# Performance work log

Hardware: AMD Instinct MI355X
Metric: run time of the kernel (lower is better)

The kernel has to match this reference:

```python
import jax, jax.numpy as jnp
import numpy as np

IN_F, OUT_F, BATCH = 4096, 11008, 8

def setup_inputs() -> dict:
    key = jax.random.key(0)
    k_x, k_s, k_sg, k_b = jax.random.split(key, 4)
    x = jax.random.normal(k_x, (BATCH, IN_F), dtype=jnp.float32)
    # stored codes in [1, 255] as in QINSCodec.encode (uint8 storage)
    stored = jax.random.randint(k_s, (OUT_F, IN_F), 1, 256, dtype=jnp.int32).astype(jnp.uint8)
    # sign in {-1, +1} (int8 storage)
    sign = (jax.random.randint(k_sg, (OUT_F, IN_F), 0, 2, dtype=jnp.int32) * 2 - 1).astype(jnp.int8)
    log_min = jnp.array([-10.0], dtype=jnp.float32)
    log_max = jnp.array([0.0], dtype=jnp.float32)
    bias = jax.random.normal(k_b, (OUT_F,), dtype=jnp.float32) * 0.02
    return {"x": x, "stored": stored, "sign": sign, "log_min": log_min, "log_max": log_max, "bias": bias}

def _decode(stored, sign, log_min, log_max):
    # QINSCodec.decode: normalized = (255 - stored)/254; w = sign * exp(log_min + normalized*(log_max-log_min))
    normalized = (255.0 - stored.astype(jnp.float32)) / 254.0
    log_w = log_min + normalized * (log_max - log_min)
    return sign.astype(jnp.float32) * jnp.exp(log_w)

def reference(x, stored, sign, log_min, log_max, bias):
    lmin = log_min[0]
    lmax = log_max[0]
    w = _decode(stored, sign, lmin, lmax)            # [OUT_F, IN_F]
    return x @ w.T + bias                            # F.linear(x, w, bias)
```

## Files before the change

kernel.cpp:

```cpp
#include <hip/hip_runtime.h>
#include <stdint.h>

#define IN_F   4096
#define OUT_F  11008
#define BATCH  8
#define RPW    4
#define WAVES  2
#define RPB    (RPW*WAVES)
#define CHUNK  256

__device__ __forceinline__ float qins_decode(int code, int sgn, float d0, float d1) {
    const float e = __builtin_amdgcn_exp2f(fmaf((float)code, d1, d0));
    const uint32_t m = ((uint32_t)sgn) & 0x80000000u;
    return __uint_as_float(__float_as_uint(e) ^ m);
}

__global__ __launch_bounds__(WAVES*64, 4)
void qins_linear_kernel(const float* __restrict__ x,
                        const int*   __restrict__ stored,
                        const int*   __restrict__ sign,
                        const float* __restrict__ log_min,
                        const float* __restrict__ log_max,
                        const float* __restrict__ bias,
                        float* __restrict__ out)
{
    const int lane = threadIdx.x & 63;
    const int wave = threadIdx.x >> 6;
    const int o0   = blockIdx.x * RPB + wave * RPW;

    const float lmin = log_min[0];
    const float lmax = log_max[0];
    const float L2E  = 1.44269504088896340736f;
    const float d1 = -(lmax - lmin) * (L2E / 254.0f);
    const float d0 = (lmin + (lmax - lmin) * (255.0f / 254.0f)) * L2E;

    float acc[RPW][BATCH];
#pragma unroll
    for (int r = 0; r < RPW; ++r)
#pragma unroll
        for (int b = 0; b < BATCH; ++b) acc[r][b] = 0.0f;

    const int ii0 = lane * 4;

    for (int i0 = 0; i0 < IN_F; i0 += CHUNK) {
        const int ii = i0 + ii0;

        float4 xr[BATCH];
#pragma unroll
        for (int b = 0; b < BATCH; ++b)
            xr[b] = *reinterpret_cast<const float4*>(x + b * IN_F + ii);

        int4 sc[RPW], sg[RPW];
#pragma unroll
        for (int r = 0; r < RPW; ++r) {
            const size_t off = (size_t)(o0 + r) * IN_F + ii;
            sc[r] = *reinterpret_cast<const int4*>(stored + off);
            sg[r] = *reinterpret_cast<const int4*>(sign + off);
        }

#pragma unroll
        for (int r = 0; r < RPW; ++r) {
            const float w0 = qins_decode(sc[r].x, sg[r].x, d0, d1);
            const float w1 = qins_decode(sc[r].y, sg[r].y, d0, d1);
            const float w2 = qins_decode(sc[r].z, sg[r].z, d0, d1);
            const float w3 = qins_decode(sc[r].w, sg[r].w, d0, d1);
#pragma unroll
            for (int b = 0; b < BATCH; ++b) {
                float a = acc[r][b];
                a = fmaf(w0, xr[b].x, a);
                a = fmaf(w1, xr[b].y, a);
                a = fmaf(w2, xr[b].z, a);
                a = fmaf(w3, xr[b].w, a);
                acc[r][b] = a;
            }
        }
    }

#pragma unroll
    for (int r = 0; r < RPW; ++r)
#pragma unroll
        for (int b = 0; b < BATCH; ++b) {
            float v = acc[r][b];
#pragma unroll
            for (int s = 32; s >= 1; s >>= 1)
                v += __shfl_xor(v, s, 64);
            acc[r][b] = v;
        }

    if (lane == 0) {
#pragma unroll
        for (int r = 0; r < RPW; ++r) {
            const float bv = bias[o0 + r];
#pragma unroll
            for (int b = 0; b < BATCH; ++b)
                out[(size_t)b * OUT_F + o0 + r] = acc[r][b] + bv;
        }
    }
}

extern "C" void kernel_launch(void* const* d_in, const int* in_sizes, int n_in,
                              void* d_out, int out_size, void* d_ws, size_t ws_size,
                              hipStream_t stream)
{
    const float* x      = (const float*)d_in[0];
    const int*   stored = (const int*)d_in[1];
    const int*   sign   = (const int*)d_in[2];
    const float* lmin   = (const float*)d_in[3];
    const float* lmax   = (const float*)d_in[4];
    const float* bias   = (const float*)d_in[5];
    float* out = (float*)d_out;

    dim3 grid(OUT_F / RPB), block(WAVES * 64);
    qins_linear_kernel<<<grid, block, 0, stream>>>(x, stored, sign, lmin, lmax, bias, out);
}
```

Before: 81.64 us.

## Split K across blocks with per-thread rows and atomic accumulation

```diff
diff --git a/kernel.cpp b/kernel.cpp
--- a/kernel.cpp
+++ b/kernel.cpp
@@ -4,29 +4,32 @@
 #define IN_F   4096
 #define OUT_F  11008
 #define BATCH  8
-#define RPW    4
-#define WAVES  2
-#define RPB    (RPW*WAVES)
-#define CHUNK  256
+#define NS     32
+#define SLICE  (IN_F / NS)
+#define ICH    16
+#define RGRPS  (OUT_F / 256)
 
-__device__ __forceinline__ float qins_decode(int code, int sgn, float d0, float d1) {
-    const float e = __builtin_amdgcn_exp2f(fmaf((float)code, d1, d0));
-    const uint32_t m = ((uint32_t)sgn) & 0x80000000u;
-    return __uint_as_float(__float_as_uint(e) ^ m);
+__global__ void qins_init(const float* __restrict__ bias, float* __restrict__ out)
+{
+    const int o = blockIdx.x * 256 + threadIdx.x;
+    const float bv = bias[o];
+#pragma unroll
+    for (int b = 0; b < BATCH; ++b)
+        out[(size_t)b * OUT_F + o] = bv;
 }
 
-__global__ __launch_bounds__(WAVES*64, 4)
-void qins_linear_kernel(const float* __restrict__ x,
-                        const int*   __restrict__ stored,
-                        const int*   __restrict__ sign,
-                        const float* __restrict__ log_min,
-                        const float* __restrict__ log_max,
-                        const float* __restrict__ bias,
-                        float* __restrict__ out)
+__global__ __launch_bounds__(256, 4)
+void qins_main(const float* __restrict__ x,
+               const int*   __restrict__ stored,
+               const int*   __restrict__ sign,
+               const float* __restrict__ log_min,
+               const float* __restrict__ log_max,
+               float* __restrict__ out)
 {
-    const int lane = threadIdx.x & 63;
-    const int wave = threadIdx.x >> 6;
-    const int o0   = blockIdx.x * RPB + wave * RPW;
+    const int rg  = blockIdx.x % RGRPS;
+    const int s   = blockIdx.x / RGRPS;
+    const int row = rg * 256 + threadIdx.x;
+    const int i0  = s * SLICE;
 
     const float lmin = log_min[0];
     const float lmax = log_max[0];
@@ -34,68 +37,49 @@
     const float d1 = -(lmax - lmin) * (L2E / 254.0f);
     const float d0 = (lmin + (lmax - lmin) * (255.0f / 254.0f)) * L2E;
 
-    float acc[RPW][BATCH];
+    float acc[BATCH];
 #pragma unroll
-    for (int r = 0; r < RPW; ++r)
+    for (int b = 0; b < BATCH; ++b) acc[b] = 0.0f;
+
+    const int base = row * IN_F + i0;
+
+    for (int it = 0; it < SLICE; it += ICH) {
+        int4 c[4], g[4];
 #pragma unroll
-        for (int b = 0; b < BATCH; ++b) acc[r][b] = 0.0f;
-
-    const int ii0 = lane * 4;
-
-    for (int i0 = 0; i0 < IN_F; i0 += CHUNK) {
-        const int ii = i0 + ii0;
-
-        float4 xr[BATCH];
-#pragma unroll
-        for (int b = 0; b < BATCH; ++b)
-            xr[b] = *reinterpret_cast<const float4*>(x + b * IN_F + ii);
-
-        int4 sc[RPW], sg[RPW];
-#pragma unroll
-        for (int r = 0; r < RPW; ++r) {
-            const size_t off = (size_t)(o0 + r) * IN_F + ii;
-            sc[r] = *reinterpret_cast<const int4*>(stored + off);
-            sg[r] = *reinterpret_cast<const int4*>(sign + off);
+        for (int q = 0; q < 4; ++q) {
+            c[q] = *reinterpret_cast<const int4*>(stored + base + it + 4 * q);
+            g[q] = *reinterpret_cast<const int4*>(sign   + base + it + 4 * q);
         }
 
 #pragma unroll
-        for (int r = 0; r < RPW; ++r) {
-            const float w0 = qins_decode(sc[r].x, sg[r].x, d0, d1);
-            const float w1 = qins_decode(sc[r].y, sg[r].y, d0, d1);
-            const float w2 = qins_decode(sc[r].z, sg[r].z, d0, d1);
-            const float w3 = qins_decode(sc[r].w, sg[r].w, d0, d1);
+        for (int q = 0; q < 4; ++q) {
+            float w[4];
+            {
+                const int cc[4] = { c[q].x, c[q].y, c[q].z, c[q].w };
+                const int gg[4] = { g[q].x, g[q].y, g[q].z, g[q].w };
+#pragma unroll
+                for (int j = 0; j < 4; ++j) {
+                    const float e = __builtin_amdgcn_exp2f(fmaf((float)cc[j], d1, d0));
+                    const uint32_t m = ((uint32_t)gg[j]) & 0x80000000u;
+                    w[j] = __uint_as_float(__float_as_uint(e) ^ m);
+                }
+            }
 #pragma unroll
             for (int b = 0; b < BATCH; ++b) {
-                float a = acc[r][b];
-                a = fmaf(w0, xr[b].x, a);
-                a = fmaf(w1, xr[b].y, a);
-                a = fmaf(w2, xr[b].z, a);
-                a = fmaf(w3, xr[b].w, a);
-                acc[r][b] = a;
+                const float* xb = x + b * IN_F + i0 + it + 4 * q;
+                float a = acc[b];
+                a = fmaf(w[0], xb[0], a);
+                a = fmaf(w[1], xb[1], a);
+                a = fmaf(w[2], xb[2], a);
+                a = fmaf(w[3], xb[3], a);
+                acc[b] = a;
             }
         }
     }
 
 #pragma unroll
-    for (int r = 0; r < RPW; ++r)
-#pragma unroll
-        for (int b = 0; b < BATCH; ++b) {
-            float v = acc[r][b];
-#pragma unroll
-            for (int s = 32; s >= 1; s >>= 1)
-                v += __shfl_xor(v, s, 64);
-            acc[r][b] = v;
-        }
-
-    if (lane == 0) {
-#pragma unroll
-        for (int r = 0; r < RPW; ++r) {
-            const float bv = bias[o0 + r];
-#pragma unroll
-            for (int b = 0; b < BATCH; ++b)
-                out[(size_t)b * OUT_F + o0 + r] = acc[r][b] + bv;
-        }
-    }
+    for (int b = 0; b < BATCH; ++b)
+        atomicAdd(out + (size_t)b * OUT_F + row, acc[b]);
 }
 
 extern "C" void kernel_launch(void* const* d_in, const int* in_sizes, int n_in,
@@ -110,6 +94,6 @@
     const float* bias   = (const float*)d_in[5];
     float* out = (float*)d_out;
 
-    dim3 grid(OUT_F / RPB), block(WAVES * 64);
-    qins_linear_kernel<<<grid, block, 0, stream>>>(x, stored, sign, lmin, lmax, bias, out);
+    qins_init<<<dim3(RGRPS), dim3(256), 0, stream>>>(bias, out);
+    qins_main<<<dim3(RGRPS * NS), dim3(256), 0, stream>>>(x, stored, sign, lmin, lmax, out);
 }
```

Measured after the change: 163.8 us. +100.7%, slower.

## Double-buffer weight loads and rebalance rows per wave with more waves

Applied to the files above, without the earlier changes.

```diff
diff --git a/kernel.cpp b/kernel.cpp
--- a/kernel.cpp
+++ b/kernel.cpp
@@ -4,8 +4,8 @@
 #define IN_F   4096
 #define OUT_F  11008
 #define BATCH  8
-#define RPW    4
-#define WAVES  2
+#define RPW    2
+#define WAVES  4
 #define RPB    (RPW*WAVES)
 #define CHUNK  256
 
@@ -14,6 +14,42 @@
     const uint32_t m = ((uint32_t)sgn) & 0x80000000u;
     return __uint_as_float(__float_as_uint(e) ^ m);
 }
+
+#define LOADW(C, G, IPOS)                                                    \
+    do {                                                                     \
+        _Pragma("unroll")                                                    \
+        for (int r = 0; r < RPW; ++r) {                                      \
+            const int off = rowbase[r] + (IPOS);                             \
+            (C)[r] = *reinterpret_cast<const int4*>(stored + off);           \
+            (G)[r] = *reinterpret_cast<const int4*>(sign + off);             \
+        }                                                                    \
+    } while (0)
+
+#define COMPUTE(C, G, IPOS)                                                  \
+    do {                                                                     \
+        float w[RPW][4];                                                     \
+        _Pragma("unroll")                                                    \
+        for (int r = 0; r < RPW; ++r) {                                      \
+            w[r][0] = qins_decode((C)[r].x, (G)[r].x, d0, d1);               \
+            w[r][1] = qins_decode((C)[r].y, (G)[r].y, d0, d1);               \
+            w[r][2] = qins_decode((C)[r].z, (G)[r].z, d0, d1);               \
+            w[r][3] = qins_decode((C)[r].w, (G)[r].w, d0, d1);               \
+        }                                                                    \
+        _Pragma("unroll")                                                    \
+        for (int b = 0; b < BATCH; ++b) {                                    \
+            const float4 t = *reinterpret_cast<const float4*>(               \
+                x + b * IN_F + (IPOS) + ii0);                                \
+            _Pragma("unroll")                                                \
+            for (int r = 0; r < RPW; ++r) {                                  \
+                float a = acc[r][b];                                         \
+                a = fmaf(w[r][0], t.x, a);                                   \
+                a = fmaf(w[r][1], t.y, a);                                   \
+                a = fmaf(w[r][2], t.z, a);                                   \
+                a = fmaf(w[r][3], t.w, a);                                   \
+                acc[r][b] = a;                                               \
+            }                                                                \
+        }                                                                    \
+    } while (0)
 
 __global__ __launch_bounds__(WAVES*64, 4)
 void qins_linear_kernel(const float* __restrict__ x,
@@ -41,40 +77,23 @@
         for (int b = 0; b < BATCH; ++b) acc[r][b] = 0.0f;
 
     const int ii0 = lane * 4;
+    int rowbase[RPW];
+#pragma unroll
+    for (int r = 0; r < RPW; ++r) rowbase[r] = (o0 + r) * IN_F + ii0;
 
-    for (int i0 = 0; i0 < IN_F; i0 += CHUNK) {
-        const int ii = i0 + ii0;
+    int4 cA[RPW], gA[RPW], cB[RPW], gB[RPW];
 
-        float4 xr[BATCH];
-#pragma unroll
-        for (int b = 0; b < BATCH; ++b)
-            xr[b] = *reinterpret_cast<const float4*>(x + b * IN_F + ii);
-
-        int4 sc[RPW], sg[RPW];
-#pragma unroll
-        for (int r = 0; r < RPW; ++r) {
-            const size_t off = (size_t)(o0 + r) * IN_F + ii;
-            sc[r] = *reinterpret_cast<const int4*>(stored + off);
-            sg[r] = *reinterpret_cast<const int4*>(sign + off);
-        }
-
-#pragma unroll
-        for (int r = 0; r < RPW; ++r) {
-            const float w0 = qins_decode(sc[r].x, sg[r].x, d0, d1);
-            const float w1 = qins_decode(sc[r].y, sg[r].y, d0, d1);
-            const float w2 = qins_decode(sc[r].z, sg[r].z, d0, d1);
-            const float w3 = qins_decode(sc[r].w, sg[r].w, d0, d1);
-#pragma unroll
-            for (int b = 0; b < BATCH; ++b) {
-                float a = acc[r][b];
-                a = fmaf(w0, xr[b].x, a);
-                a = fmaf(w1, xr[b].y, a);
-                a = fmaf(w2, xr[b].z, a);
-                a = fmaf(w3, xr[b].w, a);
-                acc[r][b] = a;
-            }
-        }
+    LOADW(cA, gA, 0);
+    int i0 = 0;
+    for (; i0 < IN_F - 2 * CHUNK; i0 += 2 * CHUNK) {
+        LOADW(cB, gB, i0 + CHUNK);
+        COMPUTE(cA, gA, i0);
+        LOADW(cA, gA, i0 + 2 * CHUNK);
+        COMPUTE(cB, gB, i0 + CHUNK);
     }
+    LOADW(cB, gB, i0 + CHUNK);
+    COMPUTE(cA, gA, i0);
+    COMPUTE(cB, gB, i0 + CHUNK);
 
 #pragma unroll
     for (int r = 0; r < RPW; ++r)
```

Measured after the change: 87.91 us. 7.7% more time.

## Assign one output row per wave with 4-wave blocks and no unrolled chunk loop

Applied to the files above, without the earlier changes.

```diff
diff --git a/kernel.cpp b/kernel.cpp
--- a/kernel.cpp
+++ b/kernel.cpp
@@ -4,10 +4,8 @@
 #define IN_F   4096
 #define OUT_F  11008
 #define BATCH  8
-#define RPW    4
-#define WAVES  2
-#define RPB    (RPW*WAVES)
 #define CHUNK  256
+#define NCHUNK (IN_F/CHUNK)
 
 __device__ __forceinline__ float qins_decode(int code, int sgn, float d0, float d1) {
     const float e = __builtin_amdgcn_exp2f(fmaf((float)code, d1, d0));
@@ -15,7 +13,7 @@
     return __uint_as_float(__float_as_uint(e) ^ m);
 }
 
-__global__ __launch_bounds__(WAVES*64, 4)
+__global__ __launch_bounds__(256, 8)
 void qins_linear_kernel(const float* __restrict__ x,
                         const int*   __restrict__ stored,
                         const int*   __restrict__ sign,
@@ -26,7 +24,7 @@
 {
     const int lane = threadIdx.x & 63;
     const int wave = threadIdx.x >> 6;
-    const int o0   = blockIdx.x * RPB + wave * RPW;
+    const int row  = blockIdx.x * 4 + wave;
 
     const float lmin = log_min[0];
     const float lmax = log_max[0];
@@ -34,67 +32,49 @@
     const float d1 = -(lmax - lmin) * (L2E / 254.0f);
     const float d0 = (lmin + (lmax - lmin) * (255.0f / 254.0f)) * L2E;
 
-    float acc[RPW][BATCH];
+    float acc[BATCH];
 #pragma unroll
-    for (int r = 0; r < RPW; ++r)
-#pragma unroll
-        for (int b = 0; b < BATCH; ++b) acc[r][b] = 0.0f;
+    for (int b = 0; b < BATCH; ++b) acc[b] = 0.0f;
 
-    const int ii0 = lane * 4;
+    const int base = row * IN_F + lane * 4;
 
+#pragma unroll 1
     for (int i0 = 0; i0 < IN_F; i0 += CHUNK) {
-        const int ii = i0 + ii0;
+        const int4 c = *reinterpret_cast<const int4*>(stored + base + i0);
+        const int4 g = *reinterpret_cast<const int4*>(sign + base + i0);
 
-        float4 xr[BATCH];
-#pragma unroll
-        for (int b = 0; b < BATCH; ++b)
-            xr[b] = *reinterpret_cast<const float4*>(x + b * IN_F + ii);
-
-        int4 sc[RPW], sg[RPW];
-#pragma unroll
-        for (int r = 0; r < RPW; ++r) {
-            const size_t off = (size_t)(o0 + r) * IN_F + ii;
-            sc[r] = *reinterpret_cast<const int4*>(stored + off);
-            sg[r] = *reinterpret_cast<const int4*>(sign + off);
-        }
+        const float w0 = qins_decode(c.x, g.x, d0, d1);
+        const float w1 = qins_decode(c.y, g.y, d0, d1);
+        const float w2 = qins_decode(c.z, g.z, d0, d1);
+        const float w3 = qins_decode(c.w, g.w, d0, d1);
 
 #pragma unroll
-        for (int r = 0; r < RPW; ++r) {
-            const float w0 = qins_decode(sc[r].x, sg[r].x, d0, d1);
-            const float w1 = qins_decode(sc[r].y, sg[r].y, d0, d1);
-            const float w2 = qins_decode(sc[r].z, sg[r].z, d0, d1);
-            const float w3 = qins_decode(sc[r].w, sg[r].w, d0, d1);
-#pragma unroll
-            for (int b = 0; b < BATCH; ++b) {
-                float a = acc[r][b];
-                a = fmaf(w0, xr[b].x, a);
-                a = fmaf(w1, xr[b].y, a);
-                a = fmaf(w2, xr[b].z, a);
-                a = fmaf(w3, xr[b].w, a);
-                acc[r][b] = a;
-            }
+        for (int b = 0; b < BATCH; ++b) {
+            const float4 t = *reinterpret_cast<const float4*>(
+                x + b * IN_F + i0 + lane * 4);
+            float a = acc[b];
+            a = fmaf(w0, t.x, a);
+            a = fmaf(w1, t.y, a);
+            a = fmaf(w2, t.z, a);
+            a = fmaf(w3, t.w, a);
+            acc[b] = a;
         }
     }
 
 #pragma unroll
-    for (int r = 0; r < RPW; ++r)
+    for (int b = 0; b < BATCH; ++b) {
+        float v = acc[b];
 #pragma unroll
-        for (int b = 0; b < BATCH; ++b) {
-            float v = acc[r][b];
-#pragma unroll
-            for (int s = 32; s >= 1; s >>= 1)
-                v += __shfl_xor(v, s, 64);
-            acc[r][b] = v;
-        }
+        for (int s = 32; s >= 1; s >>= 1)
+            v += __shfl_xor(v, s, 64);
+        acc[b] = v;
+    }
 
     if (lane == 0) {
+        const float bv = bias[row];
 #pragma unroll
-        for (int r = 0; r < RPW; ++r) {
-            const float bv = bias[o0 + r];
-#pragma unroll
-            for (int b = 0; b < BATCH; ++b)
-                out[(size_t)b * OUT_F + o0 + r] = acc[r][b] + bv;
-        }
+        for (int b = 0; b < BATCH; ++b)
+            out[(size_t)b * OUT_F + row] = acc[b] + bv;
     }
 }
 
@@ -110,6 +90,6 @@
     const float* bias   = (const float*)d_in[5];
     float* out = (float*)d_out;
 
-    dim3 grid(OUT_F / RPB), block(WAVES * 64);
+    dim3 grid(OUT_F / 4), block(256);
     qins_linear_kernel<<<grid, block, 0, stream>>>(x, stored, sign, lmin, lmax, bias, out);
 }
```

After: 107.3 us. 31.4% more time.
